# Kernel optimization log

Hardware: AMD Instinct MI355X
Metric: run time of the kernel (lower is better)

Reference implementation:

```python
import jax, jax.numpy as jnp
import numpy as np
from jax import lax

L = 32          # lattice side
H = 128         # net_width / hidden_size
B = 512         # batch_size
EPS = 1e-8


def setup_inputs() -> dict:
    key = jax.random.key(0)
    k0, k1, k2, k3, k4 = jax.random.split(key, 5)
    # binary spin configurations in {0., 1.}
    samples = jnp.round(jax.random.uniform(k0, (B, L, L))).astype(jnp.float32)
    s1 = 1.0 / np.sqrt(H + 2)
    # per-cell linear1 weights: input = cat([x(2), h(H)]) -> H
    W1 = jax.random.uniform(k1, (L * L, H, H + 2), minval=-s1, maxval=s1, dtype=jnp.float32)
    b1 = jax.random.uniform(k2, (L * L, H), minval=-s1, maxval=s1, dtype=jnp.float32)
    sf = 1.0 / np.sqrt(H)
    # per-cell fc head: H -> 1
    Wf = jax.random.uniform(k3, (L * L, H), minval=-sf, maxval=sf, dtype=jnp.float32)
    bf = jax.random.uniform(k4, (L * L,), minval=-sf, maxval=sf, dtype=jnp.float32)
    return {"samples": samples, "W1": W1, "b1": b1, "Wf": Wf, "bf": bf}


def _log_prob(samples, W1, b1, Wf, bf):
    Bsz = samples.shape[0]
    dt = samples.dtype
    W1 = W1.reshape(L, L, H, H + 2)
    b1 = b1.reshape(L, L, H)
    Wf = Wf.reshape(L, L, H)
    bf = bf.reshape(L, L)

    rows = jnp.transpose(samples, (1, 0, 2))                       # (L, B, L)
    prev = jnp.concatenate([jnp.zeros((1, Bsz, L), dt), rows[:-1]], axis=0)  # row above (x_v); zeros for row 0
    parity = (jnp.arange(L) % 2) == 1                              # odd rows scan right-to-left (zigzag)

    def row_step(h_v, xs):
        cur, pv, p, Wr, br, wfr, bfr = xs
        # reorder everything into visitation order (reverse for odd rows)
        cur_o = jnp.where(p, cur[:, ::-1], cur)     # (B, L) current-row spins / mask
        pv_o = jnp.where(p, pv[:, ::-1], pv)        # (B, L) spins of row above (x_v)
        hv_o = jnp.where(p, h_v[::-1], h_v)         # (L, B, H) vertical hidden states
        Wr_o = jnp.where(p, Wr[::-1], Wr)
        br_o = jnp.where(p, br[::-1], br)
        wf_o = jnp.where(p, wfr[::-1], wfr)
        bf_o = jnp.where(p, bfr[::-1], bfr)
        # horizontal input x_h = previously visited spin in this row (0 at row start)
        xh = jnp.concatenate([jnp.zeros((Bsz, 1), dt), cur_o[:, :-1]], axis=1)  # (B, L)

        def cell(h_h, cxs):
            xh_j, xv_j, m_j, hv_j, W, b, wf, bfs = cxs
            xh_s = jnp.stack([xh_j, 1.0 - xh_j], axis=1)   # (B, 2)
            xv_s = jnp.stack([xv_j, 1.0 - xv_j], axis=1)   # (B, 2)
            # linear1 applied to both (x_h,h_h) and (x_v,h_v); linear2 is unused in the original forward
            inp = jnp.concatenate([xh_s, h_h], axis=1) + jnp.concatenate([xv_s, hv_j], axis=1)  # (B, H+2)
            h = jnp.tanh(inp @ W.T + 2.0 * b)              # (B, H)
            x_hat = jax.nn.sigmoid(h @ wf + bfs)           # (B,)
            lp = jnp.log(x_hat + EPS) * m_j + jnp.log(1.0 - x_hat + EPS) * (1.0 - m_j)
            return h, (h, lp)

        cxs = (xh.T, pv_o.T, cur_o.T, hv_o, Wr_o, br_o, wf_o, bf_o)
        _, (hs, lps) = lax.scan(cell, jnp.zeros((Bsz, H), dt), cxs)
        h_v_new = jnp.where(p, hs[::-1], hs)               # back to raw column order
        return h_v_new, lps.sum(axis=0)                    # (B,) row log-prob

    h_v0 = jnp.zeros((L, Bsz, H), dt)
    _, row_lps = lax.scan(row_step, h_v0, (rows, prev, parity, W1, b1, Wf, bf))
    return row_lps.sum(axis=0)                             # (B,)


def reference(samples, W1, b1, Wf, bf):
    return _log_prob(samples, W1, b1, Wf, bf)
```

## Files before the change

kernel.cpp:

```cpp
#include <hip/hip_runtime.h>
#include <math.h>
#include <stdint.h>

#define Lr 32
#define Hh 128
#define NCELL (Lr * Lr)
#define NEPS 1e-8f
#define CELLB 33792

typedef _Float16 f16;
typedef f16 h2 __attribute__((ext_vector_type(2)));
typedef uint32_t u32;
typedef u32 u32x4 __attribute__((ext_vector_type(4)));
typedef u32 u32x2 __attribute__((ext_vector_type(2)));

__device__ __forceinline__ void bar_lds() {
    asm volatile("s_waitcnt lgkmcnt(0)\n\ts_barrier" ::: "memory");
}

template<int CTRL>
__device__ __forceinline__ float dpp_get(float x) {
    return __int_as_float(__builtin_amdgcn_update_dpp(
        0, __float_as_int(x), CTRL, 0xf, 0xf, true));
}

__device__ __forceinline__ float rlane(float x, int l) {
    return __int_as_float(__builtin_amdgcn_readlane(__float_as_int(x), l));
}

__device__ __forceinline__ float dot2(h2 a, h2 b, float c) {
    return __builtin_amdgcn_fdot2(a, b, c, false);
}

__device__ __forceinline__ h2 bch2(u32 v) {
    union { u32 u; h2 h; } cv; cv.u = v; return cv.h;
}
__device__ __forceinline__ float h16(u32 w, int hi) {
    union { unsigned short u; f16 h; } c;
    c.u = (unsigned short)(hi ? (w >> 16) : (w & 0xffff));
    return (float)c.h;
}

__device__ __forceinline__ float fast_tanh(float x) {
    x = fminf(9.f, fmaxf(-9.f, x));
    const float e = __expf(2.f * x);
    return 1.f - 2.f / (e + 1.f);
}

__device__ __forceinline__ int cell_of(int s) {
    const int i = s >> 5, jj = s & 31;
    const int c = (i & 1) ? (Lr - 1 - jj) : jj;
    return i * Lr + c;
}

__global__ __launch_bounds__(256)
void transpose_w(const float* __restrict__ W1, const float* __restrict__ b1,
                 const float* __restrict__ Wf, char* __restrict__ Wt) {
    __shared__ float tile[Hh * 130];
    const int cell = blockIdx.x;
    const float* src = W1 + (size_t)cell * (Hh * 130);
    for (int idx = threadIdx.x; idx < Hh * 130; idx += 256)
        tile[idx] = src[idx];
    __syncthreads();
    char* dst = Wt + (size_t)cell * CELLB;
    const int t = threadIdx.x, kk = t >> 1, hf = t & 1;
    for (int q4 = 0; q4 < 8; ++q4) {
        union { u32x4 v; f16 h[8]; } o;
        for (int j = 0; j < 4; ++j) {
            const int p = hf * 32 + q4 * 4 + j;
            o.h[2 * j]     = (f16)tile[kk * 130 + 2 + 2 * p];
            o.h[2 * j + 1] = (f16)tile[kk * 130 + 3 + 2 * p];
        }
        *(u32x4*)(dst + q4 * 4096 + t * 16) = o.v;
    }
    if (t < Hh) {
        union { u32x2 v; f16 h[4]; } o;
        const float w0 = tile[t * 130 + 0], w1 = tile[t * 130 + 1];
        const float bb = 2.f * b1[cell * Hh + t];
        o.h[0] = (f16)(2.f * w1 + bb);
        o.h[1] = (f16)(w0 + w1 + bb);
        o.h[2] = (f16)(2.f * w0 + bb);
        o.h[3] = (f16)Wf[cell * Hh + t];
        *(u32x2*)(dst + 32768 + t * 8) = o.v;
    }
}

__global__ __launch_bounds__(256, 2)
void rnn2d(const float* __restrict__ samples,
           const char* __restrict__ Wt,
           const float* __restrict__ bfv,
           float* __restrict__ out)
{
    __shared__ __align__(16) h2  inp[2][64];
    __shared__ __align__(16) f16 hvh[Lr * Hh];
    __shared__ float smp[NCELL];
    __shared__ float bfs[NCELL];
    __shared__ float fp_[2][4];
    __shared__ int   sidx[2];
    __shared__ float lpb[2];

    const int t    = threadIdx.x;
    const int k    = t >> 1;
    const int half = t & 1;
    const int w    = t >> 6;
    const int b    = blockIdx.x;

    u32 vc[8], vt;
    for (int q4 = 0; q4 < 8; ++q4) vc[q4] = (u32)(q4 * 4096 + t * 16);
    vt = (u32)(32768 + k * 8);

    {
        f16* z1 = (f16*)inp;
        for (int idx = t; idx < 2 * 64 * 2; idx += 256) z1[idx] = (f16)0.f;
        f16* z2 = (f16*)hvh;
        for (int idx = t; idx < Lr * Hh; idx += 256) z2[idx] = (f16)0.f;
        for (int idx = t; idx < NCELL; idx += 256) {
            smp[idx] = samples[(size_t)b * NCELL + idx];
            bfs[idx] = bfv[idx];
        }
        if (t == 0) sidx[0] = 0;
    }
    float lp = 0.f;

    u32x4 A0,A1,A2,A3,A4,A5,A6,A7, B0,B1,B2,B3,B4,B5,B6,B7;
    u32x4 C0,C1,C2,C3,C4,C5,C6,C7, D0,D1,D2,D3,D4,D5,D6,D7;
    u32x2 TA, TB, TC, TD;

#define ISSUE(S, W0,W1_,W2_,W3_,W4_,W5_,W6_,W7_, TT)                        \
    {                                                                       \
        const int s_ = ((S) < NCELL) ? (S) : 0;   \
        const char* cb_ = Wt + (size_t)cell_of(s_) * CELLB;                 \
        asm volatile("global_load_dwordx4 %0, %1, %2" : "=v"(W0)  : "v"(vc[0]), "s"(cb_)); \
        asm volatile("global_load_dwordx4 %0, %1, %2" : "=v"(W1_) : "v"(vc[1]), "s"(cb_)); \
        asm volatile("global_load_dwordx4 %0, %1, %2" : "=v"(W2_) : "v"(vc[2]), "s"(cb_)); \
        asm volatile("global_load_dwordx4 %0, %1, %2" : "=v"(W3_) : "v"(vc[3]), "s"(cb_)); \
        asm volatile("global_load_dwordx4 %0, %1, %2" : "=v"(W4_) : "v"(vc[4]), "s"(cb_)); \
        asm volatile("global_load_dwordx4 %0, %1, %2" : "=v"(W5_) : "v"(vc[5]), "s"(cb_)); \
        asm volatile("global_load_dwordx4 %0, %1, %2" : "=v"(W6_) : "v"(vc[6]), "s"(cb_)); \
        asm volatile("global_load_dwordx4 %0, %1, %2" : "=v"(W7_) : "v"(vc[7]), "s"(cb_)); \
        asm volatile("global_load_dwordx2 %0, %1, %2" : "=v"(TT)  : "v"(vt),    "s"(cb_)); \
    }

#define WAITP()                                                             \
    asm volatile("s_waitcnt vmcnt(18)" ::: "memory");                       \
    __builtin_amdgcn_sched_barrier(0);

#define DOT4(WQ, QQ, Q4)                                                    \
    {                                                                       \
        const u32x4 v_ = (WQ);                                              \
        const uint4 xa_ = *(const uint4*)&inp[QQ][half * 32 + (Q4) * 4];    \
        a00 = dot2(bch2(v_.x), bch2(xa_.x), a00);                           \
        a01 = dot2(bch2(v_.y), bch2(xa_.y), a01);                           \
        a02 = dot2(bch2(v_.z), bch2(xa_.z), a02);                           \
        a03 = dot2(bch2(v_.w), bch2(xa_.w), a03);                           \
    }

#define PROC(S, Q, W0,W1_,W2_,W3_,W4_,W5_,W6_,W7_, TT)                      \
    {                                                                       \
        const int i_ = (S) >> 5, j_ = (S) & 31;                             \
        const int c_ = (i_ & 1) ? (Lr - 1 - j_) : j_;                       \
        const int sn_ = ((S) + 1 < NCELL) ? (S) + 1 : (S);                  \
        const int in_ = sn_ >> 5, jn_ = sn_ & 31;                           \
        const int cn_ = (in_ & 1) ? (Lr - 1 - jn_) : jn_;                   \
        const float hvn = (float)hvh[cn_ * Hh + k];                         \
        \
        if (((t & 63) == 4) && (w < 2) && (S) > 0) {                        \
            const int cp_ = cell_of((S) - 1);                               \
            const float z_ = fp_[Q][0] + fp_[Q][1]                          \
                           + fp_[Q][2] + fp_[Q][3] + bfs[cp_];              \
            const float xh_ = 1.f / (1.f + __expf(-z_));                    \
            const float m_ = smp[cp_];                                      \
            lp += (w == 0) ? __logf(xh_ + NEPS) * m_                        \
                           : __logf(1.f - xh_ + NEPS) * (1.f - m_);         \
        }                                                                   \
        \
        float a00=0.f,a01=0.f,a02=0.f,a03=0.f;                              \
        DOT4(W0,  Q, 0) DOT4(W1_, Q, 1)                                     \
        DOT4(W2_, Q, 2) DOT4(W3_, Q, 3)                                     \
        DOT4(W4_, Q, 4) DOT4(W5_, Q, 5)                                     \
        DOT4(W6_, Q, 6) DOT4(W7_, Q, 7)                                     \
        \
        const int sx = sidx[Q];                                             \
        const float t0_ = h16(TT.x, 0), t1_ = h16(TT.x, 1);                 \
        const float t2_ = h16(TT.y, 0), wfv = h16(TT.y, 1);                 \
        float sp = (sx == 2) ? t2_ : ((sx == 1) ? t1_ : t0_);               \
        if (half) sp = 0.f;                                                 \
        float s0 = ((a00 + a01) + (a02 + a03)) + sp;                        \
        s0 += dpp_get<0xB1>(s0);    \
        const float h0 = fast_tanh(s0);                                     \
         \
        float f0 = h0 * wfv;                                                \
        f0 += dpp_get<0x4E>(f0);                                            \
        f0 += dpp_get<0x141>(f0);                                           \
        f0 += dpp_get<0x140>(f0);                                           \
        f0 = f0 + rlane(f0, 16) + rlane(f0, 32) + rlane(f0, 48);            \
        if ((S) + 1 < NCELL) {                                              \
            const float v0 = ((jn_ == 0) ? 0.f : h0)                        \
                           + ((cn_ == c_) ? h0 : hvn);                      \
            const float v0p = dpp_get<0x4E>(v0);     \
            if ((t & 3) == 0) {                                             \
                h2 u0; u0.x = (f16)v0; u0.y = (f16)v0p;                     \
                inp[(Q) ^ 1][t >> 2] = u0;                                  \
            }                                                               \
            if (t == 0) {                                                   \
                const float xh0 = (jn_ == 0) ? 0.f : smp[i_ * Lr + c_];     \
                const float xv0 = (in_ == 0) ? 0.f                          \
                                             : smp[(in_ - 1) * Lr + cn_];   \
                sidx[(Q) ^ 1] = (int)(xh0 + xv0);                           \
            }                                                               \
        }                                                                   \
        hvh[c_ * Hh + k] = (f16)h0;           \
        if ((t & 63) == 0) fp_[(Q) ^ 1][w] = f0;                            \
        bar_lds();        \
    }

    ISSUE(0, A0,A1,A2,A3,A4,A5,A6,A7, TA);
    ISSUE(1, B0,B1,B2,B3,B4,B5,B6,B7, TB);
    __syncthreads();

    for (int s = 0; s < NCELL; s += 4) {
        ISSUE(s + 2, C0,C1,C2,C3,C4,C5,C6,C7, TC); WAITP();
        PROC(s,     0, A0,A1,A2,A3,A4,A5,A6,A7, TA);
        ISSUE(s + 3, D0,D1,D2,D3,D4,D5,D6,D7, TD); WAITP();
        PROC(s + 1, 1, B0,B1,B2,B3,B4,B5,B6,B7, TB);
        ISSUE(s + 4, A0,A1,A2,A3,A4,A5,A6,A7, TA); WAITP();
        PROC(s + 2, 0, C0,C1,C2,C3,C4,C5,C6,C7, TC);
        ISSUE(s + 5, B0,B1,B2,B3,B4,B5,B6,B7, TB); WAITP();
        PROC(s + 3, 1, D0,D1,D2,D3,D4,D5,D6,D7, TD);
    }
#undef ISSUE
#undef WAITP
#undef DOT4
#undef PROC

    if (((t & 63) == 4) && (w < 2)) {
        const int cp_ = cell_of(NCELL - 1);
        const float z_ = fp_[0][0] + fp_[0][1] + fp_[0][2] + fp_[0][3]
                       + bfs[cp_];
        const float xh_ = 1.f / (1.f + __expf(-z_));
        const float m_ = smp[cp_];
        lp += (w == 0) ? __logf(xh_ + NEPS) * m_
                       : __logf(1.f - xh_ + NEPS) * (1.f - m_);
        lpb[w] = lp;
    }
    __syncthreads();
    if (t == 0) out[b] = lpb[0] + lpb[1];
}

extern "C" void kernel_launch(void* const* d_in, const int* in_sizes, int n_in,
                              void* d_out, int out_size, void* d_ws, size_t ws_size,
                              hipStream_t stream) {
    const float* samples = (const float*)d_in[0];
    const float* W1      = (const float*)d_in[1];
    const float* b1      = (const float*)d_in[2];
    const float* Wf      = (const float*)d_in[3];
    const float* bf      = (const float*)d_in[4];
    float* outp = (float*)d_out;
    char* Wt = (char*)d_ws;

    transpose_w<<<1024, 256, 0, stream>>>(W1, b1, Wf, Wt);
    rnn2d<<<512, 256, 0, stream>>>(samples, Wt, bf, outp);
}
```

Before: 960.4 us.

## Split each hidden unit across four lanes with 512-thread blocks

Each hidden unit's dot product is now spread over four lanes instead of two. Blocks grow to 512 threads and each thread holds half as many weight registers. The weight-transpose layout, DPP reductions, input staging, fp_ partial-sum array and log-prob waves change to match. The aim is shorter per-cell latency in the serial recurrence, at the cost of more cross-lane reduction steps, a shuffle, and a barrier across 8 waves instead of 4.

Result: slower. 1.040 ms (+8.3%).

```diff
diff --git a/kernel.cpp b/kernel.cpp
--- a/kernel.cpp
+++ b/kernel.cpp
@@ -63,15 +63,17 @@
         tile[idx] = src[idx];
     __syncthreads();
     char* dst = Wt + (size_t)cell * CELLB;
-    const int t = threadIdx.x, kk = t >> 1, hf = t & 1;
-    for (int q4 = 0; q4 < 8; ++q4) {
+    const int t = threadIdx.x;
+    for (int idx = t; idx < 2048; idx += 256) {
+        const int c4 = idx >> 9, tt = idx & 511;
+        const int kk = tt >> 2, q = tt & 3;
         union { u32x4 v; f16 h[8]; } o;
         for (int j = 0; j < 4; ++j) {
-            const int p = hf * 32 + q4 * 4 + j;
+            const int p = q * 16 + c4 * 4 + j;
             o.h[2 * j]     = (f16)tile[kk * 130 + 2 + 2 * p];
             o.h[2 * j + 1] = (f16)tile[kk * 130 + 3 + 2 * p];
         }
-        *(u32x4*)(dst + q4 * 4096 + t * 16) = o.v;
+        *(u32x4*)(dst + c4 * 8192 + tt * 16) = o.v;
     }
     if (t < Hh) {
         union { u32x2 v; f16 h[4]; } o;
@@ -85,7 +87,7 @@
     }
 }
 
-__global__ __launch_bounds__(256, 2)
+__global__ __launch_bounds__(512, 4)
 void rnn2d(const float* __restrict__ samples,
            const char* __restrict__ Wt,
            const float* __restrict__ bfv,
@@ -95,26 +97,26 @@
     __shared__ __align__(16) f16 hvh[Lr * Hh];
     __shared__ float smp[NCELL];
     __shared__ float bfs[NCELL];
-    __shared__ float fp_[2][4];
+    __shared__ __align__(16) float fp_[2][8];
     __shared__ int   sidx[2];
     __shared__ float lpb[2];
 
-    const int t    = threadIdx.x;
-    const int k    = t >> 1;
-    const int half = t & 1;
-    const int w    = t >> 6;
-    const int b    = blockIdx.x;
-
-    u32 vc[8], vt;
-    for (int q4 = 0; q4 < 8; ++q4) vc[q4] = (u32)(q4 * 4096 + t * 16);
+    const int t = threadIdx.x;
+    const int k = t >> 2;
+    const int q = t & 3;
+    const int w = t >> 6;
+    const int b = blockIdx.x;
+
+    u32 vc[4], vt;
+    for (int c4 = 0; c4 < 4; ++c4) vc[c4] = (u32)(c4 * 8192 + t * 16);
     vt = (u32)(32768 + k * 8);
 
     {
         f16* z1 = (f16*)inp;
-        for (int idx = t; idx < 2 * 64 * 2; idx += 256) z1[idx] = (f16)0.f;
+        for (int idx = t; idx < 2 * 64 * 2; idx += 512) z1[idx] = (f16)0.f;
         f16* z2 = (f16*)hvh;
-        for (int idx = t; idx < Lr * Hh; idx += 256) z2[idx] = (f16)0.f;
-        for (int idx = t; idx < NCELL; idx += 256) {
+        for (int idx = t; idx < Lr * Hh; idx += 512) z2[idx] = (f16)0.f;
+        for (int idx = t; idx < NCELL; idx += 512) {
             smp[idx] = samples[(size_t)b * NCELL + idx];
             bfs[idx] = bfv[idx];
         }
@@ -122,11 +124,10 @@
     }
     float lp = 0.f;
 
-    u32x4 A0,A1,A2,A3,A4,A5,A6,A7, B0,B1,B2,B3,B4,B5,B6,B7;
-    u32x4 C0,C1,C2,C3,C4,C5,C6,C7, D0,D1,D2,D3,D4,D5,D6,D7;
+    u32x4 A0,A1,A2,A3, B0,B1,B2,B3, C0,C1,C2,C3, D0,D1,D2,D3;
     u32x2 TA, TB, TC, TD;
 
-#define ISSUE(S, W0,W1_,W2_,W3_,W4_,W5_,W6_,W7_, TT)                        \
+#define ISSUE(S, W0,W1_,W2_,W3_, TT)                                        \
     {                                                                       \
         const int s_ = ((S) < NCELL) ? (S) : 0;   \
         const char* cb_ = Wt + (size_t)cell_of(s_) * CELLB;                 \
@@ -134,28 +135,24 @@
         asm volatile("global_load_dwordx4 %0, %1, %2" : "=v"(W1_) : "v"(vc[1]), "s"(cb_)); \
         asm volatile("global_load_dwordx4 %0, %1, %2" : "=v"(W2_) : "v"(vc[2]), "s"(cb_)); \
         asm volatile("global_load_dwordx4 %0, %1, %2" : "=v"(W3_) : "v"(vc[3]), "s"(cb_)); \
-        asm volatile("global_load_dwordx4 %0, %1, %2" : "=v"(W4_) : "v"(vc[4]), "s"(cb_)); \
-        asm volatile("global_load_dwordx4 %0, %1, %2" : "=v"(W5_) : "v"(vc[5]), "s"(cb_)); \
-        asm volatile("global_load_dwordx4 %0, %1, %2" : "=v"(W6_) : "v"(vc[6]), "s"(cb_)); \
-        asm volatile("global_load_dwordx4 %0, %1, %2" : "=v"(W7_) : "v"(vc[7]), "s"(cb_)); \
         asm volatile("global_load_dwordx2 %0, %1, %2" : "=v"(TT)  : "v"(vt),    "s"(cb_)); \
     }
 
 #define WAITP()                                                             \
-    asm volatile("s_waitcnt vmcnt(18)" ::: "memory");                       \
+    asm volatile("s_waitcnt vmcnt(10)" ::: "memory");                       \
     __builtin_amdgcn_sched_barrier(0);
 
-#define DOT4(WQ, QQ, Q4)                                                    \
+#define DOT4(WQ, QQ, C4)                                                    \
     {                                                                       \
         const u32x4 v_ = (WQ);                                              \
-        const uint4 xa_ = *(const uint4*)&inp[QQ][half * 32 + (Q4) * 4];    \
+        const uint4 xa_ = *(const uint4*)&inp[QQ][q * 16 + (C4) * 4];       \
         a00 = dot2(bch2(v_.x), bch2(xa_.x), a00);                           \
         a01 = dot2(bch2(v_.y), bch2(xa_.y), a01);                           \
         a02 = dot2(bch2(v_.z), bch2(xa_.z), a02);                           \
         a03 = dot2(bch2(v_.w), bch2(xa_.w), a03);                           \
     }
 
-#define PROC(S, Q, W0,W1_,W2_,W3_,W4_,W5_,W6_,W7_, TT)                      \
+#define PROC(S, Q, W0,W1_,W2_,W3_, TT)                                      \
     {                                                                       \
         const int i_ = (S) >> 5, j_ = (S) & 31;                             \
         const int c_ = (i_ & 1) ? (Lr - 1 - j_) : j_;                       \
@@ -163,44 +160,45 @@
         const int in_ = sn_ >> 5, jn_ = sn_ & 31;                           \
         const int cn_ = (in_ & 1) ? (Lr - 1 - jn_) : jn_;                   \
         const float hvn = (float)hvh[cn_ * Hh + k];                         \
-        \
-        if (((t & 63) == 4) && (w < 2) && (S) > 0) {                        \
+           \
+                       \
+        if (((t & 63) == 4) && (w == 4 || w == 5) && (S) > 0) {             \
             const int cp_ = cell_of((S) - 1);                               \
-            const float z_ = fp_[Q][0] + fp_[Q][1]                          \
-                           + fp_[Q][2] + fp_[Q][3] + bfs[cp_];              \
+            const float4 fa_ = *(const float4*)&fp_[Q][0];                  \
+            const float4 fb_ = *(const float4*)&fp_[Q][4];                  \
+            const float z_ = ((fa_.x + fa_.y) + (fa_.z + fa_.w))            \
+                           + ((fb_.x + fb_.y) + (fb_.z + fb_.w)) + bfs[cp_];\
             const float xh_ = 1.f / (1.f + __expf(-z_));                    \
             const float m_ = smp[cp_];                                      \
-            lp += (w == 0) ? __logf(xh_ + NEPS) * m_                        \
+            lp += (w == 4) ? __logf(xh_ + NEPS) * m_                        \
                            : __logf(1.f - xh_ + NEPS) * (1.f - m_);         \
         }                                                                   \
-        \
-        float a00=0.f,a01=0.f,a02=0.f,a03=0.f;                              \
+           \
+        float a00 = 0.f, a01 = 0.f, a02 = 0.f, a03 = 0.f;                   \
         DOT4(W0,  Q, 0) DOT4(W1_, Q, 1)                                     \
         DOT4(W2_, Q, 2) DOT4(W3_, Q, 3)                                     \
-        DOT4(W4_, Q, 4) DOT4(W5_, Q, 5)                                     \
-        DOT4(W6_, Q, 6) DOT4(W7_, Q, 7)                                     \
-        \
+        float s0 = (a00 + a01) + (a02 + a03);                               \
+        s0 += dpp_get<0xB1>(s0);                    \
+        s0 += dpp_get<0x4E>(s0);   \
+                     \
         const int sx = sidx[Q];                                             \
         const float t0_ = h16(TT.x, 0), t1_ = h16(TT.x, 1);                 \
         const float t2_ = h16(TT.y, 0), wfv = h16(TT.y, 1);                 \
-        float sp = (sx == 2) ? t2_ : ((sx == 1) ? t1_ : t0_);               \
-        if (half) sp = 0.f;                                                 \
-        float s0 = ((a00 + a01) + (a02 + a03)) + sp;                        \
-        s0 += dpp_get<0xB1>(s0);    \
+        s0 += (sx == 2) ? t2_ : ((sx == 1) ? t1_ : t0_);                    \
         const float h0 = fast_tanh(s0);                                     \
-         \
+            \
+           \
         float f0 = h0 * wfv;                                                \
-        f0 += dpp_get<0x4E>(f0);                                            \
         f0 += dpp_get<0x141>(f0);                                           \
         f0 += dpp_get<0x140>(f0);                                           \
         f0 = f0 + rlane(f0, 16) + rlane(f0, 32) + rlane(f0, 48);            \
         if ((S) + 1 < NCELL) {                                              \
             const float v0 = ((jn_ == 0) ? 0.f : h0)                        \
                            + ((cn_ == c_) ? h0 : hvn);                      \
-            const float v0p = dpp_get<0x4E>(v0);     \
-            if ((t & 3) == 0) {                                             \
+            const float v0p = __shfl_down(v0, 4);    \
+            if ((t & 7) == 0) {                                             \
                 h2 u0; u0.x = (f16)v0; u0.y = (f16)v0p;                     \
-                inp[(Q) ^ 1][t >> 2] = u0;                                  \
+                inp[(Q) ^ 1][t >> 3] = u0;                                  \
             }                                                               \
             if (t == 0) {                                                   \
                 const float xh0 = (jn_ == 0) ? 0.f : smp[i_ * Lr + c_];     \
@@ -209,39 +207,41 @@
                 sidx[(Q) ^ 1] = (int)(xh0 + xv0);                           \
             }                                                               \
         }                                                                   \
-        hvh[c_ * Hh + k] = (f16)h0;           \
+        if ((t & 3) == 0) hvh[c_ * Hh + k] = (f16)h0;    \
         if ((t & 63) == 0) fp_[(Q) ^ 1][w] = f0;                            \
         bar_lds();        \
     }
 
-    ISSUE(0, A0,A1,A2,A3,A4,A5,A6,A7, TA);
-    ISSUE(1, B0,B1,B2,B3,B4,B5,B6,B7, TB);
+    ISSUE(0, A0,A1,A2,A3, TA);
+    ISSUE(1, B0,B1,B2,B3, TB);
     __syncthreads();
 
     for (int s = 0; s < NCELL; s += 4) {
-        ISSUE(s + 2, C0,C1,C2,C3,C4,C5,C6,C7, TC); WAITP();
-        PROC(s,     0, A0,A1,A2,A3,A4,A5,A6,A7, TA);
-        ISSUE(s + 3, D0,D1,D2,D3,D4,D5,D6,D7, TD); WAITP();
-        PROC(s + 1, 1, B0,B1,B2,B3,B4,B5,B6,B7, TB);
-        ISSUE(s + 4, A0,A1,A2,A3,A4,A5,A6,A7, TA); WAITP();
-        PROC(s + 2, 0, C0,C1,C2,C3,C4,C5,C6,C7, TC);
-        ISSUE(s + 5, B0,B1,B2,B3,B4,B5,B6,B7, TB); WAITP();
-        PROC(s + 3, 1, D0,D1,D2,D3,D4,D5,D6,D7, TD);
+        ISSUE(s + 2, C0,C1,C2,C3, TC); WAITP();
+        PROC(s,     0, A0,A1,A2,A3, TA);
+        ISSUE(s + 3, D0,D1,D2,D3, TD); WAITP();
+        PROC(s + 1, 1, B0,B1,B2,B3, TB);
+        ISSUE(s + 4, A0,A1,A2,A3, TA); WAITP();
+        PROC(s + 2, 0, C0,C1,C2,C3, TC);
+        ISSUE(s + 5, B0,B1,B2,B3, TB); WAITP();
+        PROC(s + 3, 1, D0,D1,D2,D3, TD);
     }
 #undef ISSUE
 #undef WAITP
 #undef DOT4
 #undef PROC
 
-    if (((t & 63) == 4) && (w < 2)) {
+    if (((t & 63) == 4) && (w == 4 || w == 5)) {
         const int cp_ = cell_of(NCELL - 1);
-        const float z_ = fp_[0][0] + fp_[0][1] + fp_[0][2] + fp_[0][3]
-                       + bfs[cp_];
+        const float4 fa_ = *(const float4*)&fp_[0][0];
+        const float4 fb_ = *(const float4*)&fp_[0][4];
+        const float z_ = ((fa_.x + fa_.y) + (fa_.z + fa_.w))
+                       + ((fb_.x + fb_.y) + (fb_.z + fb_.w)) + bfs[cp_];
         const float xh_ = 1.f / (1.f + __expf(-z_));
         const float m_ = smp[cp_];
-        lp += (w == 0) ? __logf(xh_ + NEPS) * m_
+        lp += (w == 4) ? __logf(xh_ + NEPS) * m_
                        : __logf(1.f - xh_ + NEPS) * (1.f - m_);
-        lpb[w] = lp;
+        lpb[w - 4] = lp;
     }
     __syncthreads();
     if (t == 0) out[b] = lpb[0] + lpb[1];
@@ -259,5 +259,5 @@
     char* Wt = (char*)d_ws;
 
     transpose_w<<<1024, 256, 0, stream>>>(W1, b1, Wf, Wt);
-    rnn2d<<<512, 256, 0, stream>>>(samples, Wt, bf, outp);
-}
+    rnn2d<<<512, 512, 0, stream>>>(samples, Wt, bf, outp);
+}
```

## Defer fc-head reduction off critical path and hoist LDS input loads

Applied to the files above, without the earlier changes.

Moves the per-cell fc-head dot-product reduction (h·wf with DPP and readlane steps) out of the serial recurrence. It now runs at the start of the next step, so it overlaps with the wait on the weight loads and the sigmoid/log work lags two cells behind, done by waves 2-3. The LDS input vector loads are hoisted ahead of the vmcnt wait, and s_setprio raises wave priority around the dot-product and tanh section. This is meant to shorten the per-cell critical path between barriers, at the cost of more register pressure and an extra epilogue sync to drain the last two cells.

New measurement: 861.5 us. -10.3%, faster.

```diff
diff --git a/kernel.cpp b/kernel.cpp
--- a/kernel.cpp
+++ b/kernel.cpp
@@ -95,7 +95,7 @@
     __shared__ __align__(16) f16 hvh[Lr * Hh];
     __shared__ float smp[NCELL];
     __shared__ float bfs[NCELL];
-    __shared__ float fp_[2][4];
+    __shared__ __align__(16) float fp_[2][4];
     __shared__ int   sidx[2];
     __shared__ float lpb[2];
 
@@ -121,6 +121,7 @@
         if (t == 0) sidx[0] = 0;
     }
     float lp = 0.f;
+    float hPrev = 0.f, wvPrev = 0.f;
 
     u32x4 A0,A1,A2,A3,A4,A5,A6,A7, B0,B1,B2,B3,B4,B5,B6,B7;
     u32x4 C0,C1,C2,C3,C4,C5,C6,C7, D0,D1,D2,D3,D4,D5,D6,D7;
@@ -141,18 +142,13 @@
         asm volatile("global_load_dwordx2 %0, %1, %2" : "=v"(TT)  : "v"(vt),    "s"(cb_)); \
     }
 
-#define WAITP()                                                             \
-    asm volatile("s_waitcnt vmcnt(18)" ::: "memory");                       \
-    __builtin_amdgcn_sched_barrier(0);
-
-#define DOT4(WQ, QQ, Q4)                                                    \
+#define DOT4R(WQ, XQ)                                                       \
     {                                                                       \
         const u32x4 v_ = (WQ);                                              \
-        const uint4 xa_ = *(const uint4*)&inp[QQ][half * 32 + (Q4) * 4];    \
-        a00 = dot2(bch2(v_.x), bch2(xa_.x), a00);                           \
-        a01 = dot2(bch2(v_.y), bch2(xa_.y), a01);                           \
-        a02 = dot2(bch2(v_.z), bch2(xa_.z), a02);                           \
-        a03 = dot2(bch2(v_.w), bch2(xa_.w), a03);                           \
+        a00 = dot2(bch2(v_.x), bch2((XQ).x), a00);                          \
+        a01 = dot2(bch2(v_.y), bch2((XQ).y), a01);                          \
+        a02 = dot2(bch2(v_.z), bch2((XQ).z), a02);                          \
+        a03 = dot2(bch2(v_.w), bch2((XQ).w), a03);                          \
     }
 
 #define PROC(S, Q, W0,W1_,W2_,W3_,W4_,W5_,W6_,W7_, TT)                      \
@@ -162,25 +158,46 @@
         const int sn_ = ((S) + 1 < NCELL) ? (S) + 1 : (S);                  \
         const int in_ = sn_ >> 5, jn_ = sn_ & 31;                           \
         const int cn_ = (in_ & 1) ? (Lr - 1 - jn_) : jn_;                   \
+        \
+        const uint4 xq0 = *(const uint4*)&inp[Q][half * 32 + 0];            \
+        const uint4 xq1 = *(const uint4*)&inp[Q][half * 32 + 4];            \
+        const uint4 xq2 = *(const uint4*)&inp[Q][half * 32 + 8];            \
+        const uint4 xq3 = *(const uint4*)&inp[Q][half * 32 + 12];           \
         const float hvn = (float)hvh[cn_ * Hh + k];                         \
+        const int sx = sidx[Q];                                             \
         \
-        if (((t & 63) == 4) && (w < 2) && (S) > 0) {                        \
-            const int cp_ = cell_of((S) - 1);                               \
-            const float z_ = fp_[Q][0] + fp_[Q][1]                          \
-                           + fp_[Q][2] + fp_[Q][3] + bfs[cp_];              \
+        if ((S) > 0) {                                                      \
+            float fP = hPrev * wvPrev;                                      \
+            fP += dpp_get<0x4E>(fP);                                        \
+            fP += dpp_get<0x141>(fP);                                       \
+            fP += dpp_get<0x140>(fP);                                       \
+            fP = fP + rlane(fP, 16) + rlane(fP, 32) + rlane(fP, 48);        \
+            if ((t & 63) == 0) fp_[((S) - 1) & 1][w] = fP;                  \
+        }                                                                   \
+        \
+                     \
+        if (((t & 63) == 4) && (w >= 2) && (S) > 1) {                       \
+            const int cp_ = cell_of((S) - 2);                               \
+            const float4 fa_ = *(const float4*)&fp_[(S) & 1][0];            \
+            const float z_ = ((fa_.x + fa_.y) + (fa_.z + fa_.w)) + bfs[cp_];\
             const float xh_ = 1.f / (1.f + __expf(-z_));                    \
             const float m_ = smp[cp_];                                      \
-            lp += (w == 0) ? __logf(xh_ + NEPS) * m_                        \
+            lp += (w == 2) ? __logf(xh_ + NEPS) * m_                        \
                            : __logf(1.f - xh_ + NEPS) * (1.f - m_);         \
         }                                                                   \
-        \
-        float a00=0.f,a01=0.f,a02=0.f,a03=0.f;                              \
-        DOT4(W0,  Q, 0) DOT4(W1_, Q, 1)                                     \
-        DOT4(W2_, Q, 2) DOT4(W3_, Q, 3)                                     \
-        DOT4(W4_, Q, 4) DOT4(W5_, Q, 5)                                     \
-        DOT4(W6_, Q, 6) DOT4(W7_, Q, 7)                                     \
-        \
-        const int sx = sidx[Q];                                             \
+              \
+        asm volatile("s_waitcnt vmcnt(18)" ::: "memory");                   \
+        __builtin_amdgcn_sched_barrier(0);                                  \
+        __builtin_amdgcn_s_setprio(1);                                      \
+        float a00 = 0.f, a01 = 0.f, a02 = 0.f, a03 = 0.f;                   \
+        DOT4R(W0,  xq0) DOT4R(W1_, xq1)                                     \
+        DOT4R(W2_, xq2) DOT4R(W3_, xq3)                                     \
+        const uint4 xq4 = *(const uint4*)&inp[Q][half * 32 + 16];           \
+        const uint4 xq5 = *(const uint4*)&inp[Q][half * 32 + 20];           \
+        const uint4 xq6 = *(const uint4*)&inp[Q][half * 32 + 24];           \
+        const uint4 xq7 = *(const uint4*)&inp[Q][half * 32 + 28];           \
+        DOT4R(W4_, xq4) DOT4R(W5_, xq5)                                     \
+        DOT4R(W6_, xq6) DOT4R(W7_, xq7)                                     \
         const float t0_ = h16(TT.x, 0), t1_ = h16(TT.x, 1);                 \
         const float t2_ = h16(TT.y, 0), wfv = h16(TT.y, 1);                 \
         float sp = (sx == 2) ? t2_ : ((sx == 1) ? t1_ : t0_);               \
@@ -188,12 +205,6 @@
         float s0 = ((a00 + a01) + (a02 + a03)) + sp;                        \
         s0 += dpp_get<0xB1>(s0);    \
         const float h0 = fast_tanh(s0);                                     \
-         \
-        float f0 = h0 * wfv;                                                \
-        f0 += dpp_get<0x4E>(f0);                                            \
-        f0 += dpp_get<0x141>(f0);                                           \
-        f0 += dpp_get<0x140>(f0);                                           \
-        f0 = f0 + rlane(f0, 16) + rlane(f0, 32) + rlane(f0, 48);            \
         if ((S) + 1 < NCELL) {                                              \
             const float v0 = ((jn_ == 0) ? 0.f : h0)                        \
                            + ((cn_ == c_) ? h0 : hvn);                      \
@@ -210,7 +221,8 @@
             }                                                               \
         }                                                                   \
         hvh[c_ * Hh + k] = (f16)h0;           \
-        if ((t & 63) == 0) fp_[(Q) ^ 1][w] = f0;                            \
+        __builtin_amdgcn_s_setprio(0);                                      \
+        hPrev = h0; wvPrev = wfv;       \
         bar_lds();        \
     }
 
@@ -219,29 +231,39 @@
     __syncthreads();
 
     for (int s = 0; s < NCELL; s += 4) {
-        ISSUE(s + 2, C0,C1,C2,C3,C4,C5,C6,C7, TC); WAITP();
+        ISSUE(s + 2, C0,C1,C2,C3,C4,C5,C6,C7, TC);
         PROC(s,     0, A0,A1,A2,A3,A4,A5,A6,A7, TA);
-        ISSUE(s + 3, D0,D1,D2,D3,D4,D5,D6,D7, TD); WAITP();
+        ISSUE(s + 3, D0,D1,D2,D3,D4,D5,D6,D7, TD);
         PROC(s + 1, 1, B0,B1,B2,B3,B4,B5,B6,B7, TB);
-        ISSUE(s + 4, A0,A1,A2,A3,A4,A5,A6,A7, TA); WAITP();
+        ISSUE(s + 4, A0,A1,A2,A3,A4,A5,A6,A7, TA);
         PROC(s + 2, 0, C0,C1,C2,C3,C4,C5,C6,C7, TC);
-        ISSUE(s + 5, B0,B1,B2,B3,B4,B5,B6,B7, TB); WAITP();
+        ISSUE(s + 5, B0,B1,B2,B3,B4,B5,B6,B7, TB);
         PROC(s + 3, 1, D0,D1,D2,D3,D4,D5,D6,D7, TD);
     }
 #undef ISSUE
-#undef WAITP
-#undef DOT4
+#undef DOT4R
 #undef PROC
 
-    if (((t & 63) == 4) && (w < 2)) {
-        const int cp_ = cell_of(NCELL - 1);
-        const float z_ = fp_[0][0] + fp_[0][1] + fp_[0][2] + fp_[0][3]
-                       + bfs[cp_];
-        const float xh_ = 1.f / (1.f + __expf(-z_));
-        const float m_ = smp[cp_];
-        lp += (w == 0) ? __logf(xh_ + NEPS) * m_
-                       : __logf(1.f - xh_ + NEPS) * (1.f - m_);
-        lpb[w] = lp;
+    {
+        float fP = hPrev * wvPrev;
+        fP += dpp_get<0x4E>(fP);
+        fP += dpp_get<0x141>(fP);
+        fP += dpp_get<0x140>(fP);
+        fP = fP + rlane(fP, 16) + rlane(fP, 32) + rlane(fP, 48);
+        if ((t & 63) == 0) fp_[1][w] = fP;
+    }
+    __syncthreads();
+    if (((t & 63) == 4) && (w >= 2)) {
+        for (int cIdx = 0; cIdx < 2; ++cIdx) {
+            const int cp_ = cell_of(NCELL - 2 + cIdx);
+            const float4 fa_ = *(const float4*)&fp_[cIdx][0];
+            const float z_ = ((fa_.x + fa_.y) + (fa_.z + fa_.w)) + bfs[cp_];
+            const float xh_ = 1.f / (1.f + __expf(-z_));
+            const float m_ = smp[cp_];
+            lp += (w == 2) ? __logf(xh_ + NEPS) * m_
+                           : __logf(1.f - xh_ + NEPS) * (1.f - m_);
+        }
+        lpb[w - 2] = lp;
     }
     __syncthreads();
     if (t == 0) out[b] = lpb[0] + lpb[1];
```
